# Kernel optimization log

Measured on AMD Instinct MI355X. Metric: run time of the kernel, lower is better.

Reference implementation:

```python
import jax, jax.numpy as jnp
import numpy as np

# Dimensions (embedding_dim must equal 2*hidden_dim for torch.stack([w, c]) to be valid)
H = 512          # hidden_dim
D2 = 2 * H       # 1024: encoder feature dim / attention dim
D4 = 4 * H       # 2048: GRU input & hidden size
E = D2           # 1024: embedding_dim
V = 32000        # vocab_size
M = 32           # query length
N = 4096         # total passage tokens
L = 64           # answer length


def setup_inputs() -> dict:
    key = jax.random.key(0)
    ks = jax.random.split(key, 16)
    def s(k, shape, scale=0.02):
        return jax.random.normal(k, shape, dtype=jnp.float32) * scale
    return {
        "h_q": s(ks[0], (M, D2), 1.0),
        "h_p": s(ks[1], (N, D2), 1.0),
        "ans_embeds": s(ks[2], (L, E), 1.0),
        "v_w": s(ks[3], (1, D2)),          # v: Linear(2H, 1, bias=False)
        "w_d_w": s(ks[4], (D2, D2)),       # w_d: Linear(2H, 2H, bias=True)
        "w_d_b": s(ks[5], (D2,)),
        "w_a_w": s(ks[6], (D2, D2)),       # w_a: Linear(2H, 2H, bias=False)
        "u_a_w": s(ks[7], (D2, D2)),       # u_a: Linear(2H, 2H, bias=False)
        "w_r_w": s(ks[8], (D2, E)),        # w_r: Linear(E, 2H, bias=False)
        "u_r_w": s(ks[9], (D2, D2)),       # u_r: Linear(2H, 2H, bias=False)
        "v_r_w": s(ks[10], (D2, D4)),      # v_r: Linear(4H, 2H, bias=False)
        "w_o_w": s(ks[11], (V, H)),        # w_o: Linear(H, V, bias=False)
        "gru_w_ih": s(ks[12], (3 * D4, D4)),
        "gru_w_hh": s(ks[13], (3 * D4, D4)),
        "gru_b_ih": s(ks[14], (3 * D4,)),
        "gru_b_hh": s(ks[15], (3 * D4,)),
    }


def reference(h_q, h_p, ans_embeds, v_w, w_d_w, w_d_b, w_a_w, u_a_w,
              w_r_w, u_r_w, v_r_w, w_o_w, gru_w_ih, gru_w_hh, gru_b_ih, gru_b_hh):
    # h = sum over all query+passage encodings: (D2,)
    h = h_q.sum(axis=0) + h_p.sum(axis=0)
    u_a_h = h @ u_a_w.T  # precompute u_a(h): (D2,)
    # initial decoder state d = tanh(w_d([h_q[0]; h_p[0]])): (2, D2)
    d0 = jnp.tanh(jnp.stack([h_q[0], h_p[0]]) @ w_d_w.T + w_d_b)

    def gru_cell(x, hprev):
        # torch nn.GRU single-step cell, hidden size D4
        gi = gru_w_ih @ x + gru_b_ih      # (3*D4,)
        gh = gru_w_hh @ hprev + gru_b_hh  # (3*D4,)
        i_r, i_z, i_n = jnp.split(gi, 3)
        h_r, h_z, h_n = jnp.split(gh, 3)
        r = jax.nn.sigmoid(i_r + h_r)
        z = jax.nn.sigmoid(i_z + h_z)
        n = jnp.tanh(i_n + r * h_n)
        return (1.0 - z) * n + z * hprev

    def step(d2, w):
        # attention pooling over the 2 rows of d2 against pooled h
        s = jnp.tanh(d2 @ w_a_w.T + u_a_h) @ v_w[0]  # (2,)
        a = jax.nn.softmax(s)
        c = a @ d2                                    # (D2,)
        x = jnp.concatenate([w, c])                   # (D4,)
        h_new = gru_cell(x, d2.reshape(-1))           # (D4,)
        r_t = w_r_w @ w + u_r_w @ c + v_r_w @ h_new   # (D2,)
        r_t = r_t.reshape(2, H).max(axis=0)           # maxout -> (H,)
        prob = jax.nn.softmax(w_o_w @ r_t)            # (V,)
        return h_new.reshape(2, D2), prob

    _, probs = jax.lax.scan(step, d0, ans_embeds)
    return probs  # (L, V)
```

## Files before the change

kernel.cpp:

```cpp
#include <hip/hip_runtime.h>
#include <math.h>

#define H 512
#define D2 1024
#define D4 2048
#define E 1024
#define V 32000
#define M 32
#define N 4096
#define L 64
#define G3 (3*D4)

#define WS_H        0
#define WS_UAH      1024
#define WS_HSEQ     2048
#define WS_GIW      135168
#define WS_RW       528384
#define WS_GH2      593920
#define WS_GIC0     606208
#define WS_GIC1     618496
#define WS_URC0     630784
#define WS_URC1     632832
#define WS_SP0      634880
#define WS_SP1      635392
#define WS_RT       635904
#define WS_ANST     668672
#define WS_BLOCKMAX WS_GIW
#define WS_WHHB     734208
#define WS_WIHCB    7025664
#define WS_END_BF   10171392

__device__ __forceinline__ float warpSum64(float v){
#pragma unroll
    for (int off = 32; off; off >>= 1) v += __shfl_xor(v, off, 64);
    return v;
}
__device__ __forceinline__ float dot4(float4 a, float4 b){
    return a.x*b.x + a.y*b.y + a.z*b.z + a.w*b.w;
}
__device__ __forceinline__ unsigned short f2bf(float f){
    unsigned u = __float_as_uint(f);
    u += 0x7fffu + ((u >> 16) & 1u);
    return (unsigned short)(u >> 16);
}
__device__ __forceinline__ float bflo(unsigned u){ return __uint_as_float(u << 16); }
__device__ __forceinline__ float bfhi(unsigned u){ return __uint_as_float(u & 0xffff0000u); }

__global__ void k_init(const float* __restrict__ ans, float* __restrict__ ws){
    int b = blockIdx.x;
    if (b < L){
        for (int j = threadIdx.x; j < E; j += blockDim.x)
            ws[WS_ANST + j*L + b] = ans[b*E + j];
    } else {
        for (int i = threadIdx.x; i < D2; i += blockDim.x) ws[WS_H + i] = 0.f;
    }
}

__global__ __launch_bounds__(256) void k_cvt(const float* __restrict__ whh,
        const float* __restrict__ wih, float* __restrict__ ws){
    size_t idx = (size_t)blockIdx.x*blockDim.x + threadIdx.x;
    size_t nthr = (size_t)gridDim.x*blockDim.x;
    ushort4* dw = (ushort4*)(ws + WS_WHHB);
    const float4* s4 = (const float4*)whh;
    for (size_t i = idx; i < (size_t)G3*D4/4; i += nthr){
        float4 v = s4[i];
        ushort4 o; o.x = f2bf(v.x); o.y = f2bf(v.y); o.z = f2bf(v.z); o.w = f2bf(v.w);
        dw[i] = o;
    }
    ushort4* dc = (ushort4*)(ws + WS_WIHCB);
    const float4* w4 = (const float4*)wih;
    for (size_t i = idx; i < (size_t)G3*D2/4; i += nthr){
        size_t row = i / (D2/4), col = i - row*(D2/4);
        float4 v = w4[row*(D4/4) + (D2/4) + col];
        ushort4 o; o.x = f2bf(v.x); o.y = f2bf(v.y); o.z = f2bf(v.z); o.w = f2bf(v.w);
        dc[i] = o;
    }
}

__global__ void k_colsum(const float* __restrict__ hq, const float* __restrict__ hp,
                         float* __restrict__ ws){
    float4 acc = {0.f,0.f,0.f,0.f};
    int tid = threadIdx.x;
    for (int r = blockIdx.x; r < M + N; r += gridDim.x){
        const float* src = (r < M) ? (hq + (size_t)r*D2) : (hp + (size_t)(r-M)*D2);
        float4 v = ((const float4*)src)[tid];
        acc.x += v.x; acc.y += v.y; acc.z += v.z; acc.w += v.w;
    }
    float* h = ws + WS_H + tid*4;
    atomicAdd(h+0, acc.x); atomicAdd(h+1, acc.y);
    atomicAdd(h+2, acc.z); atomicAdd(h+3, acc.w);
}

__global__ __launch_bounds__(256) void k_uah_d0(
        const float* __restrict__ uaw, const float* __restrict__ wdw,
        const float* __restrict__ wdb, const float* __restrict__ hq,
        const float* __restrict__ hp, float* __restrict__ ws){
    int wid = blockIdx.x * (blockDim.x >> 6) + (threadIdx.x >> 6);
    int lane = threadIdx.x & 63;
    const float* Wrow; const float* x;
    if (wid < D2){ Wrow = uaw + (size_t)wid*D2; x = ws + WS_H; }
    else {
        int i = (wid - D2) & 1023;
        int r = (wid - D2) >> 10;
        Wrow = wdw + (size_t)i*D2;
        x = r ? hp : hq;
    }
    const float4* W4 = (const float4*)Wrow;
    const float4* x4 = (const float4*)x;
    float acc = 0.f;
#pragma unroll
    for (int m = 0; m < 4; m++){
        int j = lane + 64*m;
        acc += dot4(W4[j], x4[j]);
    }
    acc = warpSum64(acc);
    if (lane == 0){
        if (wid < D2) ws[WS_UAH + wid] = acc;
        else {
            int i = (wid - D2) & 1023, r = (wid - D2) >> 10;
            ws[WS_HSEQ + r*D2 + i] = tanhf(acc + wdb[i]);
        }
    }
}

__global__ __launch_bounds__(256) void k_pregemm(
        const float* __restrict__ wih, const float* __restrict__ bih,
        const float* __restrict__ wrw, float* __restrict__ ws){
    __shared__ float aR[32][68];
    __shared__ float b_s[64][68];
    int tid = threadIdx.x;
    int blk = blockIdx.x;
    bool isW = blk < 192;
    const float* src = isW ? wih : wrw;
    size_t stride = isW ? D4 : D2;
    int rbase = isW ? blk*32 : (blk-192)*32;
    int t0 = (tid & 15) * 4;
    int rg = (tid >> 4) * 2;
    float acc[4][2];
#pragma unroll
    for (int i = 0; i < 4; i++){ acc[i][0] = 0.f; acc[i][1] = 0.f; }

    const float* ansT = ws + WS_ANST;
    for (int kc = 0; kc < 1024; kc += 64){
        __syncthreads();
#pragma unroll
        for (int it = 0; it < 2; it++){
            int idx = it*256 + tid;
            int row = idx >> 4;
            int kq  = (idx & 15) * 4;
            float4 w = *(const float4*)(src + (size_t)(rbase + row)*stride + kc + kq);
            *(float4*)&aR[row][kq] = w;
        }
#pragma unroll
        for (int it = 0; it < 4; it++){
            int idx = it*256 + tid;
            int k = idx >> 4;
            int c4 = (idx & 15) * 4;
            *(float4*)&b_s[k][c4] = *(const float4*)(ansT + (size_t)(kc + k)*L + c4);
        }
        __syncthreads();
#pragma unroll 4
        for (int k = 0; k < 64; k++){
            float4 bb = *(float4*)&b_s[k][t0];
            float a0r = aR[rg][k], a1r = aR[rg+1][k];
            acc[0][0] += bb.x*a0r; acc[0][1] += bb.x*a1r;
            acc[1][0] += bb.y*a0r; acc[1][1] += bb.y*a1r;
            acc[2][0] += bb.z*a0r; acc[2][1] += bb.z*a1r;
            acc[3][0] += bb.w*a0r; acc[3][1] += bb.w*a1r;
        }
    }
#pragma unroll
    for (int i = 0; i < 4; i++){
#pragma unroll
        for (int j = 0; j < 2; j++){
            int r = rbase + rg + j;
            if (isW) ws[WS_GIW + (size_t)(t0+i)*G3 + r] = acc[i][j] + bih[r];
            else     ws[WS_RW  + (size_t)(t0+i)*D2 + r] = acc[i][j];
        }
    }
}

#define STEP_BLOCKS 256
#define STEP_THREADS 1024
#define NWAVES (STEP_BLOCKS*16)
__global__ __launch_bounds__(1024) void k_step(
        const float* __restrict__ whh, const float* __restrict__ bhh,
        const float* __restrict__ wih, const float* __restrict__ waw,
        const float* __restrict__ vw,  const float* __restrict__ urw,
        const float* __restrict__ vrw, float* __restrict__ ws, int t, int use_bf){
    __shared__ float4 h4s[D4/4];
    __shared__ float red[16];
    __shared__ float sa[2];
    float* h_lds = (float*)h4s;
    int tid = threadIdx.x, lane = tid & 63, wv = tid >> 6;
    int par = t & 1, pprev = par ^ 1;

    if (t >= 1){
        if (wv < 8){
            float x = ws[(wv < 4 ? WS_SP0 : WS_SP1) + pprev*256 + (wv & 3)*64 + lane];
            x = warpSum64(x);
            if (lane == 0) red[wv] = x;
        }
        __syncthreads();
        if (tid == 0){
            float s0 = red[0]+red[1]+red[2]+red[3];
            float s1 = red[4]+red[5]+red[6]+red[7];
            float mx = fmaxf(s0, s1);
            float e0 = expf(s0-mx), e1 = expf(s1-mx);
            sa[0] = e0/(e0+e1); sa[1] = e1/(e0+e1);
        }
        __syncthreads();
    }
    float a0 = (t >= 1) ? sa[0] : 0.f;
    float a1 = (t >= 1) ? sa[1] : 0.f;

    if (t == 0){
        for (int i = tid; i < D4; i += STEP_THREADS) h_lds[i] = ws[WS_HSEQ + i];
    } else {
        const float* hprev = ws + WS_HSEQ + (size_t)(t-1)*D4;
        const float* giw = ws + WS_GIW + (size_t)(t-1)*G3;
        const float* gh  = ws + WS_GH2  + pprev*G3;
        const float* g0  = ws + WS_GIC0 + pprev*G3;
        const float* g1  = ws + WS_GIC1 + pprev*G3;
        for (int k = tid; k < D4; k += STEP_THREADS){
            float gir = giw[k]      + a0*g0[k]      + a1*g1[k];
            float giz = giw[k+D4]   + a0*g0[k+D4]   + a1*g1[k+D4];
            float gin = giw[k+2*D4] + a0*g0[k+2*D4] + a1*g1[k+2*D4];
            float rr = 1.f/(1.f + expf(-(gir + gh[k])));
            float zz = 1.f/(1.f + expf(-(giz + gh[k+D4])));
            float nn = tanhf(gin + rr*gh[k+2*D4]);
            float hv = (1.f - zz)*nn + zz*hprev[k];
            h_lds[k] = hv;
            if (blockIdx.x == 0) ws[WS_HSEQ + (size_t)t*D4 + k] = hv;
        }
    }
    __syncthreads();

    const float4* h4 = (const float4*)h_lds;
    int gw = blockIdx.x*16 + wv;
    for (int task = gw; task < 14080; task += NWAVES){
        if (task < 512){
            if (t < 1) continue;
            int h = task;
            const float4* V1 = (const float4*)(vrw + (size_t)h*D4);
            const float4* V2 = (const float4*)(vrw + (size_t)(h+H)*D4);
            float acc1 = 0.f, acc2 = 0.f;
#pragma unroll
            for (int m = 0; m < 8; m++){
                int j = lane + 64*m;
                float4 hv = h4[j];
                acc1 += dot4(V1[j], hv);
                acc2 += dot4(V2[j], hv);
            }
            acc1 = warpSum64(acc1); acc2 = warpSum64(acc2);
            if (lane == 0){
                float r1 = ws[WS_RW + (size_t)(t-1)*D2 + h]
                         + acc1 + a0*ws[WS_URC0 + pprev*D2 + h]
                                + a1*ws[WS_URC1 + pprev*D2 + h];
                float r2 = ws[WS_RW + (size_t)(t-1)*D2 + h + H]
                         + acc2 + a0*ws[WS_URC0 + pprev*D2 + h + H]
                                + a1*ws[WS_URC1 + pprev*D2 + h + H];
                ws[WS_RT + (size_t)h*L + (t-1)] = fmaxf(r1, r2);
            }
        } else if (task < 768){
            if (t >= L) continue;
            int g = task - 512;
            float p0 = 0.f, p1 = 0.f;
            for (int ii = 0; ii < 4; ii++){
                int i = g*4 + ii;
                const float4* W4 = (const float4*)(waw + (size_t)i*D2);
                float ac0 = 0.f, ac1 = 0.f;
#pragma unroll
                for (int m = 0; m < 4; m++){
                    int j = lane + 64*m;
                    float4 w = W4[j];
                    ac0 += dot4(w, h4[j]);
                    ac1 += dot4(w, h4[256 + j]);
                }
                ac0 = warpSum64(ac0); ac1 = warpSum64(ac1);
                if (lane == 0){
                    float u = ws[WS_UAH + i], vv = vw[i];
                    p0 += vv * tanhf(ac0 + u);
                    p1 += vv * tanhf(ac1 + u);
                }
            }
            if (lane == 0){
                ws[WS_SP0 + par*256 + g] = p0;
                ws[WS_SP1 + par*256 + g] = p1;
            }
        } else if (task < 1792){
            if (t >= L) continue;
            int i = task - 768;
            const float4* U4 = (const float4*)(urw + (size_t)i*D2);
            float ac0 = 0.f, ac1 = 0.f;
#pragma unroll
            for (int m = 0; m < 4; m++){
                int j = lane + 64*m;
                float4 u = U4[j];
                ac0 += dot4(u, h4[j]);
                ac1 += dot4(u, h4[256 + j]);
            }
            ac0 = warpSum64(ac0); ac1 = warpSum64(ac1);
            if (lane == 0){
                ws[WS_URC0 + par*D2 + i] = ac0;
                ws[WS_URC1 + par*D2 + i] = ac1;
            }
        } else if (task < 7936){
            if (t >= L) continue;
            int k = task - 1792;
            float acc = 0.f;
            if (use_bf){
                const unsigned short* Wr = (const unsigned short*)(ws + WS_WHHB) + (size_t)k*D4;
#pragma unroll
                for (int m = 0; m < 4; m++){
                    int e = m*512 + lane*8;
                    uint4 w = *(const uint4*)(Wr + e);
                    float4 ha = h4[e>>2], hb = h4[(e>>2)+1];
                    acc += bflo(w.x)*ha.x + bfhi(w.x)*ha.y
                         + bflo(w.y)*ha.z + bfhi(w.y)*ha.w
                         + bflo(w.z)*hb.x + bfhi(w.z)*hb.y
                         + bflo(w.w)*hb.z + bfhi(w.w)*hb.w;
                }
            } else {
                const float4* W4 = (const float4*)(whh + (size_t)k*D4);
#pragma unroll
                for (int m = 0; m < 8; m++){
                    int j = lane + 64*m;
                    acc += dot4(W4[j], h4[j]);
                }
            }
            acc = warpSum64(acc);
            if (lane == 0) ws[WS_GH2 + par*G3 + k] = acc + bhh[k];
        } else {
            if (t >= L) continue;
            int k = task - 7936;
            float ac0 = 0.f, ac1 = 0.f;
            if (use_bf){
                const unsigned short* Wr = (const unsigned short*)(ws + WS_WIHCB) + (size_t)k*D2;
#pragma unroll
                for (int m = 0; m < 2; m++){
                    int e = m*512 + lane*8;
                    uint4 w = *(const uint4*)(Wr + e);
                    float4 ha = h4[e>>2],       hb = h4[(e>>2)+1];
                    float4 hc = h4[256+(e>>2)], hd = h4[256+(e>>2)+1];
                    float f0 = bflo(w.x), f1 = bfhi(w.x), f2 = bflo(w.y), f3 = bfhi(w.y);
                    float f4 = bflo(w.z), f5 = bfhi(w.z), f6 = bflo(w.w), f7 = bfhi(w.w);
                    ac0 += f0*ha.x + f1*ha.y + f2*ha.z + f3*ha.w
                         + f4*hb.x + f5*hb.y + f6*hb.z + f7*hb.w;
                    ac1 += f0*hc.x + f1*hc.y + f2*hc.z + f3*hc.w
                         + f4*hd.x + f5*hd.y + f6*hd.z + f7*hd.w;
                }
            } else {
                const float4* W4 = (const float4*)(wih + (size_t)k*D4 + D2);
#pragma unroll
                for (int m = 0; m < 4; m++){
                    int j = lane + 64*m;
                    float4 w = W4[j];
                    ac0 += dot4(w, h4[j]);
                    ac1 += dot4(w, h4[256 + j]);
                }
            }
            ac0 = warpSum64(ac0); ac1 = warpSum64(ac1);
            if (lane == 0){
                ws[WS_GIC0 + par*G3 + k] = ac0;
                ws[WS_GIC1 + par*G3 + k] = ac1;
            }
        }
    }
}

__global__ __launch_bounds__(256) void k_logits(const float* __restrict__ wo,
        float* __restrict__ out, float* __restrict__ ws){
    __shared__ float a_s[64][132];
    __shared__ float b_s[64][68];
    __shared__ float lmax[64][16];
    int tid = threadIdx.x;
    int vbase = blockIdx.x * 128;
    int tg = tid & 15;
    int vg = tid >> 4;
    int t0 = tg * 4, v0 = vg * 8;
    float acc[4][8];
#pragma unroll
    for (int i = 0; i < 4; i++)
#pragma unroll
        for (int j = 0; j < 8; j++) acc[i][j] = 0.f;

    const float* rT = ws + WS_RT;
    for (int kc = 0; kc < 512; kc += 64){
        __syncthreads();
        {
            int col = (tid & 15) * 4;
            int rbase = tid >> 4;
#pragma unroll
            for (int it = 0; it < 8; it++){
                int r = it*16 + rbase;
                float4 w = *(const float4*)(wo + (size_t)(vbase + r)*H + kc + col);
                a_s[col+0][r] = w.x; a_s[col+1][r] = w.y;
                a_s[col+2][r] = w.z; a_s[col+3][r] = w.w;
            }
#pragma unroll
            for (int it = 0; it < 4; it++){
                int idx = it*256 + tid;
                int k = idx >> 4;
                int c4 = (idx & 15) * 4;
                *(float4*)&b_s[k][c4] = *(const float4*)(rT + (size_t)(kc + k)*L + c4);
            }
        }
        __syncthreads();
#pragma unroll 4
        for (int k = 0; k < 64; k++){
            float4 bb = *(float4*)&b_s[k][t0];
            float4 aa = *(float4*)&a_s[k][v0];
            float4 ab = *(float4*)&a_s[k][v0+4];
            float bv[4] = {bb.x, bb.y, bb.z, bb.w};
            float av[8] = {aa.x, aa.y, aa.z, aa.w, ab.x, ab.y, ab.z, ab.w};
#pragma unroll
            for (int i = 0; i < 4; i++)
#pragma unroll
                for (int j = 0; j < 8; j++) acc[i][j] += bv[i]*av[j];
        }
    }
#pragma unroll
    for (int i = 0; i < 4; i++){
        float m = acc[i][0];
#pragma unroll
        for (int j = 1; j < 8; j++) m = fmaxf(m, acc[i][j]);
        lmax[t0+i][vg] = m;
        float4 o1 = {acc[i][0], acc[i][1], acc[i][2], acc[i][3]};
        float4 o2 = {acc[i][4], acc[i][5], acc[i][6], acc[i][7]};
        float* dst = out + (size_t)(t0+i)*V + vbase + v0;
        *(float4*)dst = o1;
        *(float4*)(dst+4) = o2;
    }
    __syncthreads();
    if (tid < 64){
        float m = lmax[tid][0];
#pragma unroll
        for (int j = 1; j < 16; j++) m = fmaxf(m, lmax[tid][j]);
        ws[WS_BLOCKMAX + (size_t)tid*256 + blockIdx.x] = m;
    }
}

__global__ __launch_bounds__(1024) void k_softmax(float* __restrict__ out,
                                                  const float* __restrict__ ws){
    __shared__ float red[16];
    __shared__ float bcast;
    int t = blockIdx.x, tid = threadIdx.x;
    int lane = tid & 63, wv = tid >> 6;
    float m = -3.402823466e38f;
    if (tid < 250) m = ws[WS_BLOCKMAX + (size_t)t*256 + tid];
#pragma unroll
    for (int off = 32; off; off >>= 1) m = fmaxf(m, __shfl_xor(m, off, 64));
    if (lane == 0) red[wv] = m;
    __syncthreads();
    if (tid == 0){
        float mm = red[0];
        for (int i = 1; i < 16; i++) mm = fmaxf(mm, red[i]);
        bcast = mm;
    }
    __syncthreads();
    float rmax = bcast;
    float* row = out + (size_t)t*V;
    float4 e[8];
    float s = 0.f;
#pragma unroll
    for (int i = 0; i < 8; i++){
        int idx = tid + i*1024;
        if (idx < V/4){
            float4 x = ((const float4*)row)[idx];
            e[i].x = expf(x.x - rmax); e[i].y = expf(x.y - rmax);
            e[i].z = expf(x.z - rmax); e[i].w = expf(x.w - rmax);
            s += e[i].x + e[i].y + e[i].z + e[i].w;
        }
    }
#pragma unroll
    for (int off = 32; off; off >>= 1) s += __shfl_xor(s, off, 64);
    if (lane == 0) red[wv] = s;
    __syncthreads();
    if (tid == 0){
        float ss = 0.f;
        for (int i = 0; i < 16; i++) ss += red[i];
        bcast = 1.f/ss;
    }
    __syncthreads();
    float inv = bcast;
#pragma unroll
    for (int i = 0; i < 8; i++){
        int idx = tid + i*1024;
        if (idx < V/4){
            float4 p = e[i];
            p.x *= inv; p.y *= inv; p.z *= inv; p.w *= inv;
            ((float4*)row)[idx] = p;
        }
    }
}

extern "C" void kernel_launch(void* const* d_in, const int* in_sizes, int n_in,
                              void* d_out, int out_size, void* d_ws, size_t ws_size,
                              hipStream_t stream){
    const float* hq  = (const float*)d_in[0];
    const float* hp  = (const float*)d_in[1];
    const float* ans = (const float*)d_in[2];
    const float* vw  = (const float*)d_in[3];
    const float* wdw = (const float*)d_in[4];
    const float* wdb = (const float*)d_in[5];
    const float* waw = (const float*)d_in[6];
    const float* uaw = (const float*)d_in[7];
    const float* wrw = (const float*)d_in[8];
    const float* urw = (const float*)d_in[9];
    const float* vrw = (const float*)d_in[10];
    const float* wo  = (const float*)d_in[11];
    const float* wih = (const float*)d_in[12];
    const float* whh = (const float*)d_in[13];
    const float* bih = (const float*)d_in[14];
    const float* bhh = (const float*)d_in[15];
    float* out = (float*)d_out;
    float* ws  = (float*)d_ws;

    int use_bf = (ws_size >= (size_t)WS_END_BF * 4) ? 1 : 0;

    k_init<<<L+1, 256, 0, stream>>>(ans, ws);
    if (use_bf) k_cvt<<<1024, 256, 0, stream>>>(whh, wih, ws);
    k_colsum<<<256, 256, 0, stream>>>(hq, hp, ws);
    k_uah_d0<<<768, 256, 0, stream>>>(uaw, wdw, wdb, hq, hp, ws);
    k_pregemm<<<224, 256, 0, stream>>>(wih, bih, wrw, ws);

    for (int t = 0; t <= L; t++)
        k_step<<<STEP_BLOCKS, STEP_THREADS, 0, stream>>>(whh, bhh, wih, waw, vw, urw, vrw, ws, t, use_bf);

    k_logits<<<250, 256, 0, stream>>>(wo, out, ws);
    k_softmax<<<64, 1024, 0, stream>>>(out, ws);
}
```

Measured before the change: 1.482 ms.

## Hoist u_r/v_r projections out of recurrent step into batched GEMM

Removes the per-step u_r·c and v_r·h matvecs from the sequential step kernel. Instead it records the attention weights and hidden states, then runs one batched GEMM over all 64 timesteps followed by a maxout kernel. This cuts the weight traffic through the serial loop, since u_r and v_r are now read once instead of 64 times. The final step launch is shrunk to one block, and three extra small kernels are added.

```diff
diff --git a/kernel.cpp b/kernel.cpp
--- a/kernel.cpp
+++ b/kernel.cpp
@@ -19,12 +19,14 @@
 #define WS_GH2      593920
 #define WS_GIC0     606208
 #define WS_GIC1     618496
-#define WS_URC0     630784
-#define WS_URC1     632832
+#define WS_AT       630784
 #define WS_SP0      634880
 #define WS_SP1      635392
 #define WS_RT       635904
 #define WS_ANST     668672
+#define WS_CT       WS_GIW
+#define WS_HST      (WS_GIW + 65536)
+#define WS_R3       (WS_GIW + 196608)
 #define WS_BLOCKMAX WS_GIW
 #define WS_WHHB     734208
 #define WS_WIHCB    7025664
@@ -183,11 +185,11 @@
 #define STEP_BLOCKS 256
 #define STEP_THREADS 1024
 #define NWAVES (STEP_BLOCKS*16)
+#define STEP_TASKS 12544
 __global__ __launch_bounds__(1024) void k_step(
         const float* __restrict__ whh, const float* __restrict__ bhh,
         const float* __restrict__ wih, const float* __restrict__ waw,
-        const float* __restrict__ vw,  const float* __restrict__ urw,
-        const float* __restrict__ vrw, float* __restrict__ ws, int t, int use_bf){
+        const float* __restrict__ vw,  float* __restrict__ ws, int t, int use_bf){
     __shared__ float4 h4s[D4/4];
     __shared__ float red[16];
     __shared__ float sa[2];
@@ -208,6 +210,10 @@
             float mx = fmaxf(s0, s1);
             float e0 = expf(s0-mx), e1 = expf(s1-mx);
             sa[0] = e0/(e0+e1); sa[1] = e1/(e0+e1);
+            if (blockIdx.x == 0){
+                ws[WS_AT + (t-1)*2]     = sa[0];
+                ws[WS_AT + (t-1)*2 + 1] = sa[1];
+            }
         }
         __syncthreads();
     }
@@ -236,35 +242,13 @@
     }
     __syncthreads();
 
+    if (t >= L) return;
+
     const float4* h4 = (const float4*)h_lds;
     int gw = blockIdx.x*16 + wv;
-    for (int task = gw; task < 14080; task += NWAVES){
-        if (task < 512){
-            if (t < 1) continue;
-            int h = task;
-            const float4* V1 = (const float4*)(vrw + (size_t)h*D4);
-            const float4* V2 = (const float4*)(vrw + (size_t)(h+H)*D4);
-            float acc1 = 0.f, acc2 = 0.f;
-#pragma unroll
-            for (int m = 0; m < 8; m++){
-                int j = lane + 64*m;
-                float4 hv = h4[j];
-                acc1 += dot4(V1[j], hv);
-                acc2 += dot4(V2[j], hv);
-            }
-            acc1 = warpSum64(acc1); acc2 = warpSum64(acc2);
-            if (lane == 0){
-                float r1 = ws[WS_RW + (size_t)(t-1)*D2 + h]
-                         + acc1 + a0*ws[WS_URC0 + pprev*D2 + h]
-                                + a1*ws[WS_URC1 + pprev*D2 + h];
-                float r2 = ws[WS_RW + (size_t)(t-1)*D2 + h + H]
-                         + acc2 + a0*ws[WS_URC0 + pprev*D2 + h + H]
-                                + a1*ws[WS_URC1 + pprev*D2 + h + H];
-                ws[WS_RT + (size_t)h*L + (t-1)] = fmaxf(r1, r2);
-            }
-        } else if (task < 768){
-            if (t >= L) continue;
-            int g = task - 512;
+    for (int task = gw; task < STEP_TASKS; task += NWAVES){
+        if (task < 256){
+            int g = task;
             float p0 = 0.f, p1 = 0.f;
             for (int ii = 0; ii < 4; ii++){
                 int i = g*4 + ii;
@@ -288,26 +272,8 @@
                 ws[WS_SP0 + par*256 + g] = p0;
                 ws[WS_SP1 + par*256 + g] = p1;
             }
-        } else if (task < 1792){
-            if (t >= L) continue;
-            int i = task - 768;
-            const float4* U4 = (const float4*)(urw + (size_t)i*D2);
-            float ac0 = 0.f, ac1 = 0.f;
-#pragma unroll
-            for (int m = 0; m < 4; m++){
-                int j = lane + 64*m;
-                float4 u = U4[j];
-                ac0 += dot4(u, h4[j]);
-                ac1 += dot4(u, h4[256 + j]);
-            }
-            ac0 = warpSum64(ac0); ac1 = warpSum64(ac1);
-            if (lane == 0){
-                ws[WS_URC0 + par*D2 + i] = ac0;
-                ws[WS_URC1 + par*D2 + i] = ac1;
-            }
-        } else if (task < 7936){
-            if (t >= L) continue;
-            int k = task - 1792;
+        } else if (task < 6400){
+            int k = task - 256;
             float acc = 0.f;
             if (use_bf){
                 const unsigned short* Wr = (const unsigned short*)(ws + WS_WHHB) + (size_t)k*D4;
@@ -332,8 +298,7 @@
             acc = warpSum64(acc);
             if (lane == 0) ws[WS_GH2 + par*G3 + k] = acc + bhh[k];
         } else {
-            if (t >= L) continue;
-            int k = task - 7936;
+            int k = task - 6400;
             float ac0 = 0.f, ac1 = 0.f;
             if (use_bf){
                 const unsigned short* Wr = (const unsigned short*)(ws + WS_WIHCB) + (size_t)k*D2;
@@ -367,6 +332,95 @@
             }
         }
     }
+}
+
+__global__ __launch_bounds__(256) void k_prep(float* __restrict__ ws){
+    int j = blockIdx.x;
+    const float* hA = ws + WS_HSEQ + (size_t)j*D4;
+    const float* hB = hA + D4;
+    float a0 = ws[WS_AT + 2*j], a1 = ws[WS_AT + 2*j + 1];
+    for (int k = threadIdx.x; k < D4; k += 256){
+        ws[WS_HST + (size_t)k*64 + j] = hB[k];
+        if (k < D2) ws[WS_CT + (size_t)k*64 + j] = a0*hA[k] + a1*hA[k + D2];
+    }
+}
+
+__global__ __launch_bounds__(512) void k_post(const float* __restrict__ urw,
+        const float* __restrict__ vrw, float* __restrict__ ws){
+    __shared__ float aR[64][68];
+    __shared__ float bS[64][68];
+    int tid = threadIdx.x;
+    int hb = blockIdx.x & 15;
+    int ks = blockIdx.x >> 4;
+    int hbase = hb * 32;
+    const float* A = (ks == 0) ? urw : vrw;
+    size_t astride = (ks == 0) ? D2 : D4;
+    int koff = (ks == 2) ? 1024 : 0;
+    const float* B = ws + ((ks == 0) ? WS_CT : WS_HST) + (size_t)koff*64;
+    int tg = tid & 15, vg = tid >> 4;
+    int t0 = tg*4;
+    int r0 = vg*2;
+    float acc[2][4];
+#pragma unroll
+    for (int j = 0; j < 2; j++){ acc[j][0]=acc[j][1]=acc[j][2]=acc[j][3]=0.f; }
+
+    for (int kc = 0; kc < 1024; kc += 64){
+        __syncthreads();
+#pragma unroll
+        for (int it = 0; it < 2; it++){
+            int idx = it*512 + tid;
+            int r = idx >> 4;
+            int kq = (idx & 15) * 4;
+            int grow = (r < 32) ? (hbase + r) : (512 + hbase + (r - 32));
+            *(float4*)&aR[r][kq] = *(const float4*)(A + (size_t)grow*astride + koff + kc + kq);
+        }
+#pragma unroll
+        for (int it = 0; it < 2; it++){
+            int idx = it*512 + tid;
+            int k = idx >> 4;
+            int c4 = (idx & 15)*4;
+            *(float4*)&bS[k][c4] = *(const float4*)(B + (size_t)(kc + k)*64 + c4);
+        }
+        __syncthreads();
+#pragma unroll 4
+        for (int k = 0; k < 64; k++){
+            float4 bb = *(float4*)&bS[k][t0];
+            float a0 = aR[r0][k], a1 = aR[r0+1][k];
+            acc[0][0]+=bb.x*a0; acc[0][1]+=bb.y*a0; acc[0][2]+=bb.z*a0; acc[0][3]+=bb.w*a0;
+            acc[1][0]+=bb.x*a1; acc[1][1]+=bb.y*a1; acc[1][2]+=bb.z*a1; acc[1][3]+=bb.w*a1;
+        }
+    }
+    float* R = ws + WS_R3 + (size_t)ks*65536;
+#pragma unroll
+    for (int j = 0; j < 2; j++){
+        int r = r0 + j;
+        int grow = (r < 32) ? (hbase + r) : (512 + hbase + (r - 32));
+        float4 o = {acc[j][0], acc[j][1], acc[j][2], acc[j][3]};
+        *(float4*)(R + (size_t)grow*64 + t0) = o;
+    }
+}
+
+__global__ __launch_bounds__(256) void k_rmax(float* __restrict__ ws){
+    int tid = threadIdx.x;
+    int h = blockIdx.x*16 + (tid >> 4);
+    int t0 = (tid & 15)*4;
+    const float* R = ws + WS_R3;
+    float4 x0 = *(const float4*)(R + (size_t)h*64 + t0);
+    float4 x1 = *(const float4*)(R + 65536 + (size_t)h*64 + t0);
+    float4 x2 = *(const float4*)(R + 131072 + (size_t)h*64 + t0);
+    float4 y0 = *(const float4*)(R + (size_t)(h+512)*64 + t0);
+    float4 y1 = *(const float4*)(R + 65536 + (size_t)(h+512)*64 + t0);
+    float4 y2 = *(const float4*)(R + 131072 + (size_t)(h+512)*64 + t0);
+    float4 o;
+    o.x = fmaxf(x0.x+x1.x+x2.x + ws[WS_RW + (size_t)(t0+0)*D2 + h],
+                y0.x+y1.x+y2.x + ws[WS_RW + (size_t)(t0+0)*D2 + h + 512]);
+    o.y = fmaxf(x0.y+x1.y+x2.y + ws[WS_RW + (size_t)(t0+1)*D2 + h],
+                y0.y+y1.y+y2.y + ws[WS_RW + (size_t)(t0+1)*D2 + h + 512]);
+    o.z = fmaxf(x0.z+x1.z+x2.z + ws[WS_RW + (size_t)(t0+2)*D2 + h],
+                y0.z+y1.z+y2.z + ws[WS_RW + (size_t)(t0+2)*D2 + h + 512]);
+    o.w = fmaxf(x0.w+x1.w+x2.w + ws[WS_RW + (size_t)(t0+3)*D2 + h],
+                y0.w+y1.w+y2.w + ws[WS_RW + (size_t)(t0+3)*D2 + h + 512]);
+    *(float4*)(ws + WS_RT + (size_t)h*L + t0) = o;
 }
 
 __global__ __launch_bounds__(256) void k_logits(const float* __restrict__ wo,
@@ -525,8 +579,13 @@
     k_uah_d0<<<768, 256, 0, stream>>>(uaw, wdw, wdb, hq, hp, ws);
     k_pregemm<<<224, 256, 0, stream>>>(wih, bih, wrw, ws);
 
-    for (int t = 0; t <= L; t++)
-        k_step<<<STEP_BLOCKS, STEP_THREADS, 0, stream>>>(whh, bhh, wih, waw, vw, urw, vrw, ws, t, use_bf);
+    for (int t = 0; t < L; t++)
+        k_step<<<STEP_BLOCKS, STEP_THREADS, 0, stream>>>(whh, bhh, wih, waw, vw, ws, t, use_bf);
+    k_step<<<1, STEP_THREADS, 0, stream>>>(whh, bhh, wih, waw, vw, ws, L, use_bf);
+
+    k_prep<<<L, 256, 0, stream>>>(ws);
+    k_post<<<48, 512, 0, stream>>>(urw, vrw, ws);
+    k_rmax<<<32, 256, 0, stream>>>(ws);
 
     k_logits<<<250, 256, 0, stream>>>(wo, out, ws);
     k_softmax<<<64, 1024, 0, stream>>>(out, ws);
```

After: 1.463 ms. No clear change (-1.2%).
